# Kernel tuning notes

Measured on AMD Instinct MI355X. Metric: run time of the kernel, lower is better.

The kernel has to match this reference:

```python
import jax, jax.numpy as jnp
import numpy as np

# AdaptiveLIF neuron constants (tau_mem=20, tau_thresh=60 from __init__)
TAU_MEM = 20.0
TAU_THRESH = 60.0
TH_BASE = 1.0      # resting threshold
TH_INC = 0.1       # threshold increment per spike (adaptation)
SG_SLOPE = 4.0     # surrogate-gradient sigmoid slope


def _spike(u):
    """Heaviside forward, sigmoid surrogate gradient (straight-through)."""
    sig = jax.nn.sigmoid(SG_SLOPE * u)
    hard = (u >= 0).astype(u.dtype)
    return jax.lax.stop_gradient(hard - sig) + sig


def setup_inputs() -> dict:
    key = jax.random.key(0)
    k1, k2, k3 = jax.random.split(key, 3)
    B, N, FIN, FOUT = 2, 8192, 128, 128
    x = jax.random.normal(k1, (B, N, FIN), dtype=jnp.float32)
    # dense adjacency, roughly row-normalized so pre-activations are O(1)
    adj = jax.random.uniform(k2, (B, N, N), dtype=jnp.float32) * (2.0 / N)
    weight = jax.random.normal(k3, (FIN, FOUT), dtype=jnp.float32) * (1.0 / np.sqrt(FIN))
    bias = jnp.zeros((FOUT,), dtype=jnp.float32)
    return {"x": x, "adj": adj, "weight": weight, "bias": bias, "time_steps": 5}


def reference(x, adj, weight, bias, time_steps):
    # support = x @ W ; output = adj @ support + b  -> constant drive I per step
    support = jnp.einsum('bnf,fg->bng', x, weight)          # [B,N,Fout]
    I = jnp.einsum('bnm,bmg->bng', adj, support) + bias     # [B,N,Fout]

    mem_decay = 1.0 - 1.0 / TAU_MEM

    # Fused recurrence: instead of materializing the repeated 4D tensor,
    # scan the adaptive-LIF state and accumulate the spike sum in-carry.
    def step(carry, _):
        v, th, acc = carry
        v = v * mem_decay + I                     # leaky integration
        s = _spike(v - th)                        # threshold crossing
        v = v * (1.0 - s)                         # reset on spike
        th = th + (TH_BASE - th) / TAU_THRESH + TH_INC * s  # adaptive threshold
        return (v, th, acc + s), None

    v0 = jnp.zeros_like(I)
    th0 = jnp.full_like(I, TH_BASE)
    acc0 = jnp.zeros_like(I)
    (_, _, acc), _ = jax.lax.scan(step, (v0, th0, acc0), None, length=time_steps)
    return acc / float(time_steps)                # mean over time -> [B,N,Fout]
```

## Files before the change

kernel.cpp:

```cpp
#include <hip/hip_runtime.h>
#include <math.h>

typedef __attribute__((ext_vector_type(8))) short short8;
typedef __attribute__((ext_vector_type(4))) float f32x4;

static __device__ __forceinline__ unsigned short f2bf(float f) {
  unsigned int u = __float_as_uint(f);
  u = u + 0x7fffu + ((u >> 16) & 1u);
  return (unsigned short)(u >> 16);
}

__global__ __launch_bounds__(256) void support_kernel(
    const float* __restrict__ x, const float* __restrict__ w,
    unsigned short* __restrict__ supT, int N) {
  __shared__ float aT[64][65];
  __shared__ float bs[64][132];

  const int tid = threadIdx.x;
  const long long r0 = (long long)blockIdx.x * 64;
  const float* Ab = x + r0 * 128;
  const int tx = tid & 15;
  const int ty = tid >> 4;

  float acc[4][8] = {};
  const int ar = tid & 63, ak = (tid >> 6) * 16;
  const int bk = tid >> 2, bc = (tid & 3) * 32;

  for (int k0 = 0; k0 < 128; k0 += 64) {
    const float4* asrc = (const float4*)(Ab + (long long)ar * 128 + k0 + ak);
    #pragma unroll
    for (int j = 0; j < 4; ++j) {
      float4 v = asrc[j];
      aT[ak + 4*j + 0][ar] = v.x;
      aT[ak + 4*j + 1][ar] = v.y;
      aT[ak + 4*j + 2][ar] = v.z;
      aT[ak + 4*j + 3][ar] = v.w;
    }
    const float4* bsrc = (const float4*)(w + (long long)(k0 + bk) * 128 + bc);
    #pragma unroll
    for (int j = 0; j < 8; ++j) *(float4*)&bs[bk][bc + 4*j] = bsrc[j];
    __syncthreads();
    #pragma unroll 16
    for (int k = 0; k < 64; ++k) {
      float a[4], b[8];
      *(float4*)a      = *(const float4*)&aT[k][ty*4];
      *(float4*)&b[0]  = *(const float4*)&bs[k][tx*8];
      *(float4*)&b[4]  = *(const float4*)&bs[k][tx*8 + 4];
      #pragma unroll
      for (int i = 0; i < 4; ++i)
        #pragma unroll
        for (int j = 0; j < 8; ++j)
          acc[i][j] = fmaf(a[i], b[j], acc[i][j]);
    }
    __syncthreads();
  }
  const int batch = (int)(r0 / N);
  const int nloc = (int)(r0 % N) + ty * 4;
  #pragma unroll
  for (int j = 0; j < 8; ++j) {
    const int col = tx * 8 + j;
    ushort4 pv;
    pv.x = f2bf(acc[0][j]); pv.y = f2bf(acc[1][j]);
    pv.z = f2bf(acc[2][j]); pv.w = f2bf(acc[3][j]);
    *(ushort4*)&supT[(size_t)batch * 128 * N + (size_t)col * N + nloc] = pv;
  }
}

#define BK2 128
#define ASTR 136

__global__ __launch_bounds__(256) void spike_gemm_kernel(
    const float* __restrict__ adj, const unsigned short* __restrict__ supT,
    const float* __restrict__ bias, const int* __restrict__ tsp,
    float* __restrict__ out, int N) {
  __shared__ __align__(16) unsigned short As[32][ASTR];

  const int tid = threadIdx.x;
  const int lane = tid & 63;
  const int wave = tid >> 6;
  const int batch = blockIdx.y;
  const int n0 = blockIdx.x * 32;

  const float* Ab = adj + ((size_t)batch * N + n0) * N;
  const unsigned short* Bb = supT + (size_t)batch * 128 * N;

  const int ar = tid >> 4;
  const int akq = tid & 15;

  const int fm = lane & 15;
  const int kg = lane >> 4;

  f32x4 acc[2][2] = {};

  const int NT = N / BK2;

  const unsigned short* bp0 = Bb + (size_t)(wave * 32 + 0 * 16 + fm) * N + kg * 8;
  const unsigned short* bp1 = Bb + (size_t)(wave * 32 + 1 * 16 + fm) * N + kg * 8;
  const float* ap0 = Ab + (size_t)ar * N + akq * 8;
  const float* ap1 = Ab + (size_t)(ar + 16) * N + akq * 8;

  uint4 bfrA[2][4], bfrB[2][4];
  float4 adjA[4], adjB[4];

  auto issueB = [&](uint4 (&dst)[2][4], int k0) {
    #pragma unroll
    for (int ks = 0; ks < 4; ++ks) {
      dst[0][ks] = *(const uint4*)(bp0 + k0 + ks * 32);
      dst[1][ks] = *(const uint4*)(bp1 + k0 + ks * 32);
    }
  };
  auto issueA = [&](float4 (&dst)[4], int k0) {
    dst[0] = *(const float4*)(ap0 + k0);
    dst[1] = *(const float4*)(ap0 + k0 + 4);
    dst[2] = *(const float4*)(ap1 + k0);
    dst[3] = *(const float4*)(ap1 + k0 + 4);
  };
  auto writeA = [&](const float4 (&s)[4]) {
    short8 v0, v1;
    v0[0] = (short)f2bf(s[0].x); v0[1] = (short)f2bf(s[0].y);
    v0[2] = (short)f2bf(s[0].z); v0[3] = (short)f2bf(s[0].w);
    v0[4] = (short)f2bf(s[1].x); v0[5] = (short)f2bf(s[1].y);
    v0[6] = (short)f2bf(s[1].z); v0[7] = (short)f2bf(s[1].w);
    v1[0] = (short)f2bf(s[2].x); v1[1] = (short)f2bf(s[2].y);
    v1[2] = (short)f2bf(s[2].z); v1[3] = (short)f2bf(s[2].w);
    v1[4] = (short)f2bf(s[3].x); v1[5] = (short)f2bf(s[3].y);
    v1[6] = (short)f2bf(s[3].z); v1[7] = (short)f2bf(s[3].w);
    *(short8*)&As[ar][akq * 8]      = v0;
    *(short8*)&As[ar + 16][akq * 8] = v1;
  };
  auto compute = [&](const uint4 (&bfr)[2][4]) {
    #pragma unroll
    for (int ks = 0; ks < 4; ++ks) {
      short8 a0 = *(const short8*)&As[fm][ks * 32 + kg * 8];
      short8 a1 = *(const short8*)&As[16 + fm][ks * 32 + kg * 8];
      #pragma unroll
      for (int ct = 0; ct < 2; ++ct) {
        short8 b = *(const short8*)&bfr[ct][ks];
        acc[0][ct] = __builtin_amdgcn_mfma_f32_16x16x32_bf16(a0, b, acc[0][ct], 0, 0, 0);
        acc[1][ct] = __builtin_amdgcn_mfma_f32_16x16x32_bf16(a1, b, acc[1][ct], 0, 0, 0);
      }
    }
  };

  issueA(adjA, 0);
  issueB(bfrA, 0);
  issueA(adjB, BK2);
  writeA(adjA);
  asm volatile("s_waitcnt lgkmcnt(0)" ::: "memory");
  __builtin_amdgcn_s_barrier();

  for (int t = 0; t < NT; t += 2) {
    {
      const int kn1 = (t + 1) * BK2;
      const int kn2 = ((t + 2) < NT ? (t + 2) : 0) * BK2;
      issueB(bfrB, kn1);
      issueA(adjA, kn2);
      compute(bfrA);
      __builtin_amdgcn_s_barrier();
      writeA(adjB);
      asm volatile("s_waitcnt lgkmcnt(0)" ::: "memory");
      __builtin_amdgcn_s_barrier();
    }
    {
      const int u = t + 1;
      const int kn1 = ((u + 1) < NT ? (u + 1) : 0) * BK2;
      const int kn2 = ((u + 2) < NT ? (u + 2) : (u + 2 - NT)) * BK2;
      issueB(bfrA, kn1);
      issueA(adjB, kn2);
      compute(bfrB);
      __builtin_amdgcn_s_barrier();
      writeA(adjA);
      asm volatile("s_waitcnt lgkmcnt(0)" ::: "memory");
      __builtin_amdgcn_s_barrier();
    }
  }

  const int T = *tsp;
  #pragma unroll
  for (int rt = 0; rt < 2; ++rt) {
    #pragma unroll
    for (int ct = 0; ct < 2; ++ct) {
      const int col = wave * 32 + ct * 16 + fm;
      const float bv = bias[col];
      #pragma unroll
      for (int i = 0; i < 4; ++i) {
        float I = acc[rt][ct][i] + bv;
        float v = 0.0f, th = 1.0f, sacc = 0.0f;
        for (int t = 0; t < T; ++t) {
          v = v * 0.95f + I;
          float u = v - th;
          float sig = 1.0f / (1.0f + expf(-4.0f * u));
          float hard = (u >= 0.0f) ? 1.0f : 0.0f;
          float s = (hard - sig) + sig;
          sacc += s;
          v = v * (1.0f - s);
          th = th + (1.0f - th) / 60.0f + 0.1f * s;
        }
        const int row = n0 + rt * 16 + kg * 4 + i;
        out[((size_t)batch * N + row) * 128 + col] = sacc / (float)T;
      }
    }
  }
}

extern "C" void kernel_launch(void* const* d_in, const int* in_sizes, int n_in,
                              void* d_out, int out_size, void* d_ws, size_t ws_size,
                              hipStream_t stream) {
  const float* x    = (const float*)d_in[0];
  const float* adj  = (const float*)d_in[1];
  const float* w    = (const float*)d_in[2];
  const float* bias = (const float*)d_in[3];
  const int*   tsp  = (const int*)d_in[4];
  float* out = (float*)d_out;
  unsigned short* supT = (unsigned short*)d_ws;

  const long long sz_x = in_sizes[0];
  const long long sz_adj = in_sizes[1];
  const int N = (int)(sz_adj / sz_x * 128);
  const int B = (int)(sz_x / ((long long)N * 128));
  const int rows = B * N;

  support_kernel<<<rows / 64, 256, 0, stream>>>(x, w, supT, N);
  spike_gemm_kernel<<<dim3(N / 32, B), 256, 0, stream>>>(adj, supT, bias, tsp, out, N);
}
```

Measured before the change: 762.9 us.

## Split adjacency GEMM along K into four slices with separate LIF reduction kernel

The adj @ support GEMM grid gains a z-dimension of four K-slices, raising the block count from 512 to 2048 to better fill the GPU. Each slice writes fp32 partial sums to workspace. A new elementwise kernel adds the four partials plus bias and runs the adaptive-LIF recurrence. This trades extra partial-sum traffic and a third kernel launch for more parallelism on the bandwidth-heavy adjacency stream.

After: 779.4 us. +2.2%, slower.

```diff
diff --git a/kernel.cpp b/kernel.cpp
--- a/kernel.cpp
+++ b/kernel.cpp
@@ -3,6 +3,10 @@
 
 typedef __attribute__((ext_vector_type(8))) short short8;
 typedef __attribute__((ext_vector_type(4))) float f32x4;
+
+#define SK 4
+#define BK2 128
+#define ASTR 136
 
 static __device__ __forceinline__ unsigned short f2bf(float f) {
   unsigned int u = __float_as_uint(f);
@@ -66,13 +70,9 @@
   }
 }
 
-#define BK2 128
-#define ASTR 136
-
 __global__ __launch_bounds__(256) void spike_gemm_kernel(
     const float* __restrict__ adj, const unsigned short* __restrict__ supT,
-    const float* __restrict__ bias, const int* __restrict__ tsp,
-    float* __restrict__ out, int N) {
+    float* __restrict__ pacc, int N) {
   __shared__ __align__(16) unsigned short As[32][ASTR];
 
   const int tid = threadIdx.x;
@@ -80,9 +80,11 @@
   const int wave = tid >> 6;
   const int batch = blockIdx.y;
   const int n0 = blockIdx.x * 32;
-
-  const float* Ab = adj + ((size_t)batch * N + n0) * N;
-  const unsigned short* Bb = supT + (size_t)batch * 128 * N;
+  const int kz = blockIdx.z;
+  const int kbase = kz * (N / SK);
+
+  const float* Ab = adj + ((size_t)batch * N + n0) * N + kbase;
+  const unsigned short* Bb = supT + (size_t)batch * 128 * N + kbase;
 
   const int ar = tid >> 4;
   const int akq = tid & 15;
@@ -92,7 +94,7 @@
 
   f32x4 acc[2][2] = {};
 
-  const int NT = N / BK2;
+  const int NT = N / (BK2 * SK);
 
   const unsigned short* bp0 = Bb + (size_t)(wave * 32 + 0 * 16 + fm) * N + kg * 8;
   const unsigned short* bp1 = Bb + (size_t)(wave * 32 + 1 * 16 + fm) * N + kg * 8;
@@ -175,32 +177,55 @@
     }
   }
 
-  const int T = *tsp;
+  float* pb = pacc + (size_t)(kz * gridDim.y + batch) * N * 128;
   #pragma unroll
   for (int rt = 0; rt < 2; ++rt) {
     #pragma unroll
     for (int ct = 0; ct < 2; ++ct) {
       const int col = wave * 32 + ct * 16 + fm;
-      const float bv = bias[col];
       #pragma unroll
       for (int i = 0; i < 4; ++i) {
-        float I = acc[rt][ct][i] + bv;
-        float v = 0.0f, th = 1.0f, sacc = 0.0f;
-        for (int t = 0; t < T; ++t) {
-          v = v * 0.95f + I;
-          float u = v - th;
-          float sig = 1.0f / (1.0f + expf(-4.0f * u));
-          float hard = (u >= 0.0f) ? 1.0f : 0.0f;
-          float s = (hard - sig) + sig;
-          sacc += s;
-          v = v * (1.0f - s);
-          th = th + (1.0f - th) / 60.0f + 0.1f * s;
-        }
         const int row = n0 + rt * 16 + kg * 4 + i;
-        out[((size_t)batch * N + row) * 128 + col] = sacc / (float)T;
+        pb[(size_t)row * 128 + col] = acc[rt][ct][i];
       }
     }
   }
+}
+
+__global__ __launch_bounds__(256) void lif_kernel(
+    const float* __restrict__ pacc, const float* __restrict__ bias,
+    const int* __restrict__ tsp, float* __restrict__ out, int slice_f4) {
+  const int idx = blockIdx.x * 256 + threadIdx.x;
+  const float4* p = (const float4*)pacc;
+  float4 s0 = p[idx];
+  float4 s1 = p[idx + (size_t)slice_f4];
+  float4 s2 = p[idx + (size_t)slice_f4 * 2];
+  float4 s3 = p[idx + (size_t)slice_f4 * 3];
+  const float4 bv = *(const float4*)&bias[(idx & 31) * 4];
+  float I[4];
+  I[0] = ((s0.x + s1.x) + s2.x) + s3.x + bv.x;
+  I[1] = ((s0.y + s1.y) + s2.y) + s3.y + bv.y;
+  I[2] = ((s0.z + s1.z) + s2.z) + s3.z + bv.z;
+  I[3] = ((s0.w + s1.w) + s2.w) + s3.w + bv.w;
+  const int T = *tsp;
+  float4 r;
+  float* rp = (float*)&r;
+  #pragma unroll
+  for (int c = 0; c < 4; ++c) {
+    float v = 0.0f, th = 1.0f, sacc = 0.0f;
+    for (int t = 0; t < T; ++t) {
+      v = v * 0.95f + I[c];
+      float u = v - th;
+      float sig = 1.0f / (1.0f + expf(-4.0f * u));
+      float hard = (u >= 0.0f) ? 1.0f : 0.0f;
+      float s = (hard - sig) + sig;
+      sacc += s;
+      v = v * (1.0f - s);
+      th = th + (1.0f - th) / 60.0f + 0.1f * s;
+    }
+    rp[c] = sacc / (float)T;
+  }
+  ((float4*)out)[idx] = r;
 }
 
 extern "C" void kernel_launch(void* const* d_in, const int* in_sizes, int n_in,
@@ -212,7 +237,6 @@
   const float* bias = (const float*)d_in[3];
   const int*   tsp  = (const int*)d_in[4];
   float* out = (float*)d_out;
-  unsigned short* supT = (unsigned short*)d_ws;
 
   const long long sz_x = in_sizes[0];
   const long long sz_adj = in_sizes[1];
@@ -220,6 +244,13 @@
   const int B = (int)(sz_x / ((long long)N * 128));
   const int rows = B * N;
 
+  unsigned short* supT = (unsigned short*)d_ws;
+  size_t supT_bytes = (size_t)B * 128 * N * 2;
+  supT_bytes = (supT_bytes + 255) & ~(size_t)255;
+  float* pacc = (float*)((char*)d_ws + supT_bytes);
+
   support_kernel<<<rows / 64, 256, 0, stream>>>(x, w, supT, N);
-  spike_gemm_kernel<<<dim3(N / 32, B), 256, 0, stream>>>(adj, supT, bias, tsp, out, N);
-}
+  spike_gemm_kernel<<<dim3(N / 32, B, SK), 256, 0, stream>>>(adj, supT, pacc, N);
+  const int slice_f4 = B * N * 32;
+  lif_kernel<<<slice_f4 / 256, 256, 0, stream>>>(pacc, bias, tsp, out, slice_f4);
+}
```
